# Kernel optimization log

Hardware: AMD Instinct MI355X
Metric: run time of the kernel (lower is better)

## Reference

```python
import jax, jax.numpy as jnp
import numpy as np
import math

D = 768; H = 8; HD = D // H; T = 1024; V = 32000; M = 10
BLOCK = 128          # flex-attention block size (sliding_window_num_blocks granularity)
TAU = 1.0            # gumbel_temp
MAXC = 10            # max middle-block visits == scan length
EPS = 1e-6
IFP = 0.95           # initial_forward_prob

def rms(x):
    return x * jax.lax.rsqrt(jnp.mean(x * x, axis=-1, keepdims=True) + EPS)

def make_rope(t):
    # Rotary.__init__: dim//4 real inv freqs + dim//4 zeros -> cos/sin of shape [t, HD//2]
    inv = (1.0 / 1024) ** jnp.linspace(0.0, 1.0, HD // 4)
    inv = jnp.concatenate([inv, jnp.zeros(HD // 4)])
    th = jnp.arange(t, dtype=jnp.float32)[:, None] * inv[None, :]
    return jnp.cos(th), jnp.sin(th)

def rope(x, cos, sin):
    # x: [1,T,H,HD]
    c = cos[None, :, None, :]; s = sin[None, :, None, :]
    x1, x2 = jnp.split(x, 2, axis=-1)
    return jnp.concatenate([x1 * c + x2 * s, -x1 * s + x2 * c], axis=-1)

def attn(x, ve, wq, wk, wv, wo, lam, cos, sin, mask):
    q = (x @ wq.T).reshape(1, T, H, HD)
    k = (x @ wk.T).reshape(1, T, H, HD)
    v = (x @ wv.T).reshape(1, T, H, HD)
    if ve is not None:
        v = lam[0] * v + lam[1] * ve.reshape(1, T, H, HD)
    else:
        v = lam[0] * v
    q = rope(rms(q), cos, sin); k = rope(rms(k), cos, sin)
    sc = jnp.einsum('bthd,bshd->bhts', q, k) * (1.0 / math.sqrt(HD))
    sc = jnp.where(mask, sc, -1e30)
    y = jnp.einsum('bhts,bshd->bthd', jax.nn.softmax(sc, axis=-1), v).reshape(1, T, D)
    return y @ wo.T

def mlp(x, fc, pr):
    return jnp.square(jax.nn.relu(x @ fc.T)) @ pr.T

def fwd(tokens, embed_w, ve_w, lm_head_w,
        in_wq, in_wk, in_wv, in_wo, in_attn_lam, in_fc, in_pr, in_lam,
        mid_wq, mid_wk, mid_wv, mid_wo, mid_attn_lam, mid_fc, mid_pr, router_w, router_b,
        out_wq, out_wk, out_wv, out_wo, out_attn_lam, out_fc, out_pr, out_lam,
        gumbel_u, window_blocks, max_block_count):
    cos, sin = make_rope(T)
    qi = jnp.arange(T)
    mask = ((qi[:, None] >= qi[None, :]) &
            ((qi[:, None] // BLOCK - qi[None, :] // BLOCK) < window_blocks))[None, None]
    x = rms(embed_w[tokens][None])     # norm(embed(inputs))
    x0 = x
    ve = ve_w[tokens][None]            # X=1 value embedding, reused for output block
    # ---- input FixedBlock ----
    h = in_lam[0] * x + in_lam[1] * x0
    h = h + attn(rms(h), ve, in_wq, in_wk, in_wv, in_wo, in_attn_lam, cos, sin, mask)
    h = h + mlp(rms(h), in_fc, in_pr)
    # ---- middle routing loop (fixed-length scan, masked once exited) ----
    g = -jnp.log(-jnp.log(gumbel_u + 1e-10) + 1e-10)  # [MAXC, M+1] gumbel noise
    mbc = jnp.float32(max_block_count)
    def step(carry, gi):
        x, cur, done, cnt = carry
        y = x + attn(rms(x), None, mid_wq[cur], mid_wk[cur], mid_wv[cur], mid_wo[cur],
                     mid_attn_lam[cur], cos, sin, mask)
        y = y + mlp(rms(y), mid_fc[cur], mid_pr[cur])
        feat = jnp.concatenate([y.mean(axis=1), jnp.stack([cnt, mbc])[None]], axis=-1)  # [1, D+2]
        logits = feat @ router_w[cur].T + router_b[cur]                                  # [1, M+1]
        route = jax.nn.softmax((logits + gi[None]) / TAU, axis=-1)
        nxt = jnp.argmax(route[0]).astype(jnp.int32)
        new_cnt = cnt + 1.0
        exit_now = (nxt == M) | (new_cnt >= mbc)
        x = jnp.where(done, x, y)
        cnt = jnp.where(done, cnt, new_cnt)
        new_done = done | exit_now
        cur = jnp.where(new_done, cur, nxt)
        return (x, cur, new_done, cnt), None
    init = (h, jnp.int32(0), jnp.bool_(False), jnp.float32(0.0))
    (x, _, _, _), _ = jax.lax.scan(step, init, g)
    # ---- output FixedBlock ----
    y = out_lam[0] * x + out_lam[1] * x0
    y = y + attn(rms(y), ve, out_wq, out_wk, out_wv, out_wo, out_attn_lam, cos, sin, mask)
    y = y + mlp(rms(y), out_fc, out_pr)
    logits = rms(y) @ lm_head_w.T
    return 30.0 * jnp.tanh(logits / 30.0)

def setup_inputs() -> dict:
    key = jax.random.key(0)
    ks = iter(jax.random.split(key, 64))
    def w(*s, std=0.02):
        return (std * jax.random.normal(next(ks), s)).astype(jnp.float32)
    rb = np.full((M, M + 1), math.log((1.0 - IFP) / M), dtype=np.float32)
    for i in range(M):
        rb[i, min(i + 1, M)] = math.log(IFP)
    inp = {
        'tokens': jax.random.randint(next(ks), (T,), 0, V, dtype=jnp.int32),
        'embed_w': w(V, D), 've_w': w(V, D), 'lm_head_w': w(V, D),
        'in_wq': w(D, D), 'in_wk': w(D, D), 'in_wv': w(D, D), 'in_wo': w(D, D),
        'in_attn_lam': jnp.array([0.5, 0.5], jnp.float32),
        'in_fc': w(4 * D, D), 'in_pr': w(D, 4 * D),
        'in_lam': jnp.array([1.0, 0.0], jnp.float32),
        'mid_wq': w(M, D, D), 'mid_wk': w(M, D, D), 'mid_wv': w(M, D, D), 'mid_wo': w(M, D, D),
        'mid_attn_lam': jnp.tile(jnp.array([0.5, 0.5], jnp.float32), (M, 1)),
        'mid_fc': w(M, 4 * D, D), 'mid_pr': w(M, D, 4 * D),
        'router_w': w(M, M + 1, D + 2, std=0.001),
        'router_b': jnp.asarray(rb),
        'out_wq': w(D, D), 'out_wk': w(D, D), 'out_wv': w(D, D), 'out_wo': w(D, D),
        'out_attn_lam': jnp.array([0.5, 0.5], jnp.float32),
        'out_fc': w(4 * D, D), 'out_pr': w(D, 4 * D),
        'out_lam': jnp.array([1.0, 0.0], jnp.float32),
        'gumbel_u': jax.random.uniform(next(ks), (MAXC, M + 1), dtype=jnp.float32),
        'window_blocks': 4,
        'max_block_count': MAXC,
    }
    return inp

def reference(tokens, embed_w, ve_w, lm_head_w,
              in_wq, in_wk, in_wv, in_wo, in_attn_lam, in_fc, in_pr, in_lam,
              mid_wq, mid_wk, mid_wv, mid_wo, mid_attn_lam, mid_fc, mid_pr, router_w, router_b,
              out_wq, out_wk, out_wv, out_wo, out_attn_lam, out_fc, out_pr, out_lam,
              gumbel_u, window_blocks, max_block_count):
    return fwd(tokens, embed_w, ve_w, lm_head_w,
               in_wq, in_wk, in_wv, in_wo, in_attn_lam, in_fc, in_pr, in_lam,
               mid_wq, mid_wk, mid_wv, mid_wo, mid_attn_lam, mid_fc, mid_pr, router_w, router_b,
               out_wq, out_wk, out_wv, out_wo, out_attn_lam, out_fc, out_pr, out_lam,
               gumbel_u, window_blocks, max_block_count)
```

## Files before the change

kernel.cpp:

```cpp
#include <hip/hip_runtime.h>
#include <hip/hip_bf16.h>

namespace {

constexpr int cT   = 1024;
constexpr int cD   = 768;
constexpr int cH   = 8;
constexpr int cHD  = 96;
constexpr int cM   = 10;
constexpr int cDff = 3072;
constexpr int cV   = 32000;
constexpr int cTD  = cT * cD;
constexpr float cEps = 1e-6f;

constexpr long oWQ = 0;
constexpr long oWK = 589824;
constexpr long oWV = 2L * 589824;
constexpr long oWO = 3L * 589824;
constexpr long oFC = 4L * 589824;
constexpr long oPR = 4L * 589824 + 2359296;
constexpr long cWTOT = 4L * 589824 + 2L * 2359296;
constexpr int cConvBlocks = (int)(cWTOT / 8 / 256);

typedef __attribute__((ext_vector_type(8))) short short8;
typedef __attribute__((ext_vector_type(4))) float f32x4;

__device__ inline short bf16r(float f) {
  union { float f; unsigned u; } x{f};
  unsigned r = (x.u + 0x7FFF + ((x.u >> 16) & 1)) >> 16;
  return (short)r;
}

__device__ inline float bf2f(short s) {
  union { unsigned u; float f; } x;
  x.u = ((unsigned)(unsigned short)s) << 16;
  return x.f;
}


__global__ void init_state_k(int* cur, int* done, float* cnt, float* feat) {
  if (threadIdx.x == 0) { *cur = 0; *done = 0; *cnt = 0.0f; }
  for (int d = threadIdx.x; d < cD; d += 256) feat[d] = 0.f;
}

__global__ void rope_pre_k(float* __restrict__ cosb, float* __restrict__ sinb) {
  int idx = blockIdx.x * blockDim.x + threadIdx.x;
  if (idx >= cT * 48) return;
  int t = idx / 48, j = idx % 48;
  float th = 0.0f;
  if (j < 24) th = (float)t * powf(1.0f / 1024.0f, (float)j / 23.0f);
  cosb[idx] = cosf(th);
  sinb[idx] = sinf(th);
}

__global__ __launch_bounds__(256) void embed_rms_k(const int* __restrict__ tok,
    const float* __restrict__ ew, const float* __restrict__ vw,
    float* __restrict__ x0, float* __restrict__ ve) {
  int t = blockIdx.x;
  int tk = tok[t];
  const float* er = ew + (size_t)tk * cD;
  const float* vr = vw + (size_t)tk * cD;
  __shared__ float red[256];
  float s = 0.f;
  for (int d = threadIdx.x; d < cD; d += 256) { float e = er[d]; s += e * e; }
  red[threadIdx.x] = s; __syncthreads();
  for (int st = 128; st; st >>= 1) { if (threadIdx.x < st) red[threadIdx.x] += red[threadIdx.x + st]; __syncthreads(); }
  float sc = rsqrtf(red[0] / cD + cEps);
  for (int d = threadIdx.x; d < cD; d += 256) {
    x0[(size_t)t * cD + d] = er[d] * sc;
    ve[(size_t)t * cD + d] = vr[d];
  }
}

__global__ __launch_bounds__(256) void rms_rows_bf(const float* __restrict__ in,
    short* __restrict__ out, const int* done) {
  if (done && *done) return;
  int t = blockIdx.x;
  const float* r = in + (size_t)t * cD;
  __shared__ float red[256];
  float s = 0.f;
  for (int d = threadIdx.x; d < cD; d += 256) { float v = r[d]; s += v * v; }
  red[threadIdx.x] = s; __syncthreads();
  for (int st = 128; st; st >>= 1) { if (threadIdx.x < st) red[threadIdx.x] += red[threadIdx.x + st]; __syncthreads(); }
  float sc = rsqrtf(red[0] / cD + cEps);
  short* o = out + (size_t)t * cD;
  for (int d = threadIdx.x; d < cD; d += 256) o[d] = bf16r(r[d] * sc);
}

__global__ void axpy_lam_k(const float* __restrict__ lam, const float* __restrict__ a,
                           const float* __restrict__ b, float* __restrict__ o, int n) {
  int i = blockIdx.x * 256 + threadIdx.x;
  if (i < n) o[i] = lam[0] * a[i] + lam[1] * b[i];
}


__global__ __launch_bounds__(256) void layer_pre_k(const float* __restrict__ s0,
    const float* __restrict__ s1, const float* __restrict__ s2, const float* __restrict__ s3,
    const float* __restrict__ s4, const float* __restrict__ s5, short* __restrict__ dst,
    const int* __restrict__ cur, const int* __restrict__ done,
    const float* __restrict__ xin, short* __restrict__ xnbf, float* __restrict__ rsum) {
  if (done && *done) return;
  const int b = blockIdx.x;
  if (b < cConvBlocks) {
    long e = ((long)b * 256 + threadIdx.x) * 8;
    long cu = cur ? (long)(*cur) : 0L;
    const float* src;
    if (e < oWK)      src = s0 + cu * 589824  + e;
    else if (e < oWV) src = s1 + cu * 589824  + (e - oWK);
    else if (e < oWO) src = s2 + cu * 589824  + (e - oWV);
    else if (e < oFC) src = s3 + cu * 589824  + (e - oWO);
    else if (e < oPR) src = s4 + cu * 2359296 + (e - oFC);
    else              src = s5 + cu * 2359296 + (e - oPR);
    float4 a0 = *(const float4*)src;
    float4 a1 = *(const float4*)(src + 4);
    short8 sv;
    sv[0]=bf16r(a0.x); sv[1]=bf16r(a0.y); sv[2]=bf16r(a0.z); sv[3]=bf16r(a0.w);
    sv[4]=bf16r(a1.x); sv[5]=bf16r(a1.y); sv[6]=bf16r(a1.z); sv[7]=bf16r(a1.w);
    *(short8*)(dst + e) = sv;
  } else {
    const int t = b - cConvBlocks;
    const float* r = xin + (size_t)t * cD;
    __shared__ float red[256];
    float s = 0.f;
    for (int d = threadIdx.x; d < cD; d += 256) { float v = r[d]; s += v * v; }
    red[threadIdx.x] = s; __syncthreads();
    for (int st = 128; st; st >>= 1) { if (threadIdx.x < st) red[threadIdx.x] += red[threadIdx.x + st]; __syncthreads(); }
    float sc = rsqrtf(red[0] / cD + cEps);
    short* o = xnbf + (size_t)t * cD;
    for (int d = threadIdx.x; d < cD; d += 256) o[d] = bf16r(r[d] * sc);
    if (threadIdx.x == 0) rsum[t] = 0.f;
  }
}

__global__ __launch_bounds__(256) void conv1_k(const float* __restrict__ src,
    short* __restrict__ dst, long nchunk) {
  long i = (long)blockIdx.x * 256 + threadIdx.x;
  if (i >= nchunk) return;
  long e = i * 8;
  float4 a0 = *(const float4*)(src + e);
  float4 a1 = *(const float4*)(src + e + 4);
  short8 sv;
  sv[0]=bf16r(a0.x); sv[1]=bf16r(a0.y); sv[2]=bf16r(a0.z); sv[3]=bf16r(a0.w);
  sv[4]=bf16r(a1.x); sv[5]=bf16r(a1.y); sv[6]=bf16r(a1.z); sv[7]=bf16r(a1.w);
  *(short8*)(dst + e) = sv;
}


__global__ __launch_bounds__(256) void qkv_k(const short* __restrict__ A,
    const short* __restrict__ Wb,
    short* __restrict__ qo, short* __restrict__ ko, short* __restrict__ vo,
    const int* __restrict__ done, const float* __restrict__ lamb,
    const int* __restrict__ cur, const float* __restrict__ vep,
    const float* __restrict__ cosb, const float* __restrict__ sinb) {
  if (done && *done) return;
  const int z = blockIdx.z;
  const short* W = Wb + (long)z * 589824L;
  const int h  = blockIdx.x;
  const int bm = blockIdx.y * 64;
  __shared__ short As[2][64][40];
  __shared__ short Bs[2][96][40];
  const int tid = threadIdx.x;
  const int w = tid >> 6, lane = tid & 63;
  const int fr = lane & 15, fg = lane >> 4;
  const int ar = tid >> 2, ac2 = (tid & 3) << 3;
  const int br1 = (256 + tid) >> 2, bc1 = ((256 + tid) & 3) << 3;

  short8 aN, bN0, bN1;
  aN  = *(const short8*)(A + (size_t)(bm + ar) * cD + ac2);
  bN0 = *(const short8*)(W + (size_t)(h * cHD + ar) * cD + ac2);
  if (tid < 128) bN1 = *(const short8*)(W + (size_t)(h * cHD + br1) * cD + bc1);
  *(short8*)&As[0][ar][ac2] = aN;
  *(short8*)&Bs[0][ar][ac2] = bN0;
  if (tid < 128) *(short8*)&Bs[0][br1][bc1] = bN1;
  __syncthreads();

  f32x4 acc[6] = {};
  int cb = 0;
  for (int kt = 0; kt < cD; kt += 32) {
    const int ktn = kt + 32;
    const bool hn = ktn < cD;
    if (hn) {
      aN  = *(const short8*)(A + (size_t)(bm + ar) * cD + ktn + ac2);
      bN0 = *(const short8*)(W + (size_t)(h * cHD + ar) * cD + ktn + ac2);
      if (tid < 128) bN1 = *(const short8*)(W + (size_t)(h * cHD + br1) * cD + ktn + bc1);
    }
    short8 af = *(const short8*)&As[cb][w * 16 + fr][fg * 8];
#pragma unroll
    for (int n = 0; n < 6; ++n) {
      short8 bf = *(const short8*)&Bs[cb][n * 16 + fr][fg * 8];
      acc[n] = __builtin_amdgcn_mfma_f32_16x16x32_bf16(af, bf, acc[n], 0, 0, 0);
    }
    if (hn) {
      *(short8*)&As[cb ^ 1][ar][ac2] = aN;
      *(short8*)&Bs[cb ^ 1][ar][ac2] = bN0;
      if (tid < 128) *(short8*)&Bs[cb ^ 1][br1][bc1] = bN1;
    }
    __syncthreads();
    cb ^= 1;
  }

  const int t0 = bm + w * 16 + fg * 4;
  if (z < 2) {
    float scl[4];
#pragma unroll
    for (int r = 0; r < 4; ++r) {
      float s = 0.f;
#pragma unroll
      for (int n = 0; n < 6; ++n) s += acc[n][r] * acc[n][r];
#pragma unroll
      for (int mm = 1; mm < 16; mm <<= 1) s += __shfl_xor(s, mm, 64);
      scl[r] = rsqrtf(s * (1.0f / 96.0f) + cEps);
    }
    short* C = (z == 0 ? qo : ko);
#pragma unroll
    for (int r = 0; r < 4; ++r) {
      int t = t0 + r;
      short* orow = C + (size_t)t * cD + h * cHD;
#pragma unroll
      for (int n = 0; n < 3; ++n) {
        int j = n * 16 + fr;
        float c = cosb[t * 48 + j], sn = sinb[t * 48 + j];
        float x1 = acc[n][r] * scl[r], x2 = acc[n + 3][r] * scl[r];
        orow[j]      = bf16r(x1 * c + x2 * sn);
        orow[j + 48] = bf16r(-x1 * sn + x2 * c);
      }
    }
  } else {
    int cu = cur ? *cur : 0;
    float l0 = lamb[2 * cu], l1 = lamb[2 * cu + 1];
#pragma unroll
    for (int r = 0; r < 4; ++r) {
      int t = t0 + r;
#pragma unroll
      for (int n = 0; n < 6; ++n) {
        float val = l0 * acc[n][r];
        if (vep) val += l1 * vep[(size_t)t * cD + h * cHD + n * 16 + fr];
        vo[(size_t)t * cD + h * cHD + n * 16 + fr] = bf16r(val);
      }
    }
  }
}


__global__ __launch_bounds__(256) void attn_f(const short* __restrict__ q,
    const short* __restrict__ k, const short* __restrict__ v, short* __restrict__ o,
    const int* __restrict__ wbp, const int* done) {
  if (done && *done) return;
  const int qb = blockIdx.x;
  const int h  = blockIdx.y;
  const int q0 = qb * 64;
  const int qb128 = q0 >> 7;
  const int wb = *wbp;
  int kb_lo = qb128 - wb + 1; if (kb_lo < 0) kb_lo = 0;

  __shared__ short Ksh[128][136];
  __shared__ short Vt[96][136];

  const int tid  = threadIdx.x;
  const int w    = tid >> 6;
  const int lane = tid & 63;
  const int fr   = lane & 15;
  const int fg   = lane >> 4;

  short8 qf[3];
  {
    const short* qrow = q + (size_t)(q0 + w * 16 + fr) * cD + h * cHD;
#pragma unroll
    for (int ks = 0; ks < 3; ++ks) qf[ks] = *(const short8*)(qrow + ks * 32 + fg * 8);
  }

  short8 rK[6], rV[6];
  auto issue = [&](int kb) {
    const int key0 = kb * 128;
#pragma unroll
    for (int c = 0; c < 6; ++c) {
      int idx = c * 256 + tid;
      int row = idx / 12, colc = (idx % 12) * 8;
      rK[c] = *(const short8*)(k + (size_t)(key0 + row) * cD + h * cHD + colc);
      rV[c] = *(const short8*)(v + (size_t)(key0 + row) * cD + h * cHD + colc);
    }
  };

  f32x4 accO[6] = {};
  float mrun[4], lrun[4];
#pragma unroll
  for (int r = 0; r < 4; ++r) { mrun[r] = -1e30f; lrun[r] = 0.f; }

  issue(kb_lo);
  for (int kb = kb_lo; kb <= qb128; ++kb) {
    __syncthreads();
#pragma unroll
    for (int c = 0; c < 6; ++c) {
      int idx = c * 256 + tid;
      int row = idx / 12, colc = (idx % 12) * 8;
      *(short8*)&Ksh[row][colc] = rK[c];
      short8 vv = rV[c];
#pragma unroll
      for (int i = 0; i < 8; ++i) Vt[colc + i][row] = vv[i];
    }
    __syncthreads();
    if (kb < qb128) issue(kb + 1);

    const int key0 = kb * 128;
    f32x4 s[8];
#pragma unroll
    for (int n = 0; n < 8; ++n) s[n] = (f32x4){0.f, 0.f, 0.f, 0.f};
#pragma unroll
    for (int ks = 0; ks < 3; ++ks) {
#pragma unroll
      for (int n = 0; n < 8; ++n) {
        short8 kf = *(const short8*)&Ksh[n * 16 + fr][ks * 32 + fg * 8];
        s[n] = __builtin_amdgcn_mfma_f32_16x16x32_bf16(qf[ks], kf, s[n], 0, 0, 0);
      }
    }

    float pmax[4] = {-1e30f, -1e30f, -1e30f, -1e30f};
#pragma unroll
    for (int n = 0; n < 8; ++n)
#pragma unroll
      for (int r = 0; r < 4; ++r) {
        float val = s[n][r] * 0.10206207261596577f;
        int key  = key0 + n * 16 + fr;
        int qrow = q0 + w * 16 + fg * 4 + r;
        if (key > qrow) val = -1e30f;
        s[n][r] = val;
        pmax[r] = fmaxf(pmax[r], val);
      }
#pragma unroll
    for (int mm = 1; mm < 16; mm <<= 1)
#pragma unroll
      for (int r = 0; r < 4; ++r) pmax[r] = fmaxf(pmax[r], __shfl_xor(pmax[r], mm, 64));
    float alpha[4], psum[4];
#pragma unroll
    for (int r = 0; r < 4; ++r) {
      float mn = fmaxf(mrun[r], pmax[r]);
      alpha[r] = __expf(mrun[r] - mn);
      mrun[r] = mn;
      psum[r] = 0.f;
    }
#pragma unroll
    for (int n = 0; n < 8; ++n)
#pragma unroll
      for (int r = 0; r < 4; ++r) {
        float p = __expf(s[n][r] - mrun[r]);
        s[n][r] = p;
        psum[r] += p;
      }
#pragma unroll
    for (int mm = 1; mm < 16; mm <<= 1)
#pragma unroll
      for (int r = 0; r < 4; ++r) psum[r] += __shfl_xor(psum[r], mm, 64);
#pragma unroll
    for (int r = 0; r < 4; ++r) lrun[r] = lrun[r] * alpha[r] + psum[r];
#pragma unroll
    for (int n = 0; n < 6; ++n) {
      f32x4 t = accO[n];
#pragma unroll
      for (int r = 0; r < 4; ++r) t[r] *= alpha[r];
      accO[n] = t;
    }

    __syncthreads();
#pragma unroll
    for (int n = 0; n < 8; ++n)
#pragma unroll
      for (int r = 0; r < 4; ++r)
        Ksh[w * 16 + fg * 4 + r][n * 16 + fr] = bf16r(s[n][r]);
    __syncthreads();

#pragma unroll
    for (int ks = 0; ks < 4; ++ks) {
      short8 pf = *(const short8*)&Ksh[w * 16 + fr][ks * 32 + fg * 8];
#pragma unroll
      for (int n = 0; n < 6; ++n) {
        short8 vf = *(const short8*)&Vt[n * 16 + fr][ks * 32 + fg * 8];
        accO[n] = __builtin_amdgcn_mfma_f32_16x16x32_bf16(pf, vf, accO[n], 0, 0, 0);
      }
    }
  }

#pragma unroll
  for (int r = 0; r < 4; ++r) {
    float inv = 1.0f / lrun[r];
    int t = q0 + w * 16 + fg * 4 + r;
#pragma unroll
    for (int n = 0; n < 6; ++n)
      o[(size_t)t * cD + h * cHD + n * 16 + fr] = bf16r(accO[n][r] * inv);
  }
}


template <int EPI, typename OT>
__global__ __launch_bounds__(256) void gemm64_k(const short* __restrict__ A,
    const short* __restrict__ W, OT* __restrict__ C, const int* __restrict__ done,
    const float* __restrict__ res, float* __restrict__ rsum, int ld, int kn, int N) {
  if (done && *done) return;
  const int bm = blockIdx.y * 64;
  const int bn = blockIdx.x * 64;
  const int k0 = blockIdx.z * kn;
  __shared__ short As[2][64][40];
  __shared__ short Bs[2][64][40];
  const int tid = threadIdx.x;
  const int wid = tid >> 6, lane = tid & 63;
  const int wr = wid >> 1, wc = wid & 1;
  const int fr = lane & 15, fg = lane >> 4;
  const int ar = tid >> 2, ac = (tid & 3) << 3;

  short8 aN = *(const short8*)(A + (size_t)(bm + ar) * ld + k0 + ac);
  short8 bN = *(const short8*)(W + (size_t)(bn + ar) * ld + k0 + ac);
  *(short8*)&As[0][ar][ac] = aN;
  *(short8*)&Bs[0][ar][ac] = bN;
  __syncthreads();

  f32x4 acc[2][2] = {};
  int cb = 0;
  for (int kt = 0; kt < kn; kt += 32) {
    const int ktn = kt + 32;
    const bool hn = ktn < kn;
    if (hn) {
      aN = *(const short8*)(A + (size_t)(bm + ar) * ld + k0 + ktn + ac);
      bN = *(const short8*)(W + (size_t)(bn + ar) * ld + k0 + ktn + ac);
    }
    short8 af[2], bfv[2];
#pragma unroll
    for (int m = 0; m < 2; ++m) af[m] = *(const short8*)&As[cb][wr * 32 + m * 16 + fr][fg * 8];
#pragma unroll
    for (int n = 0; n < 2; ++n) bfv[n] = *(const short8*)&Bs[cb][wc * 32 + n * 16 + fr][fg * 8];
#pragma unroll
    for (int m = 0; m < 2; ++m)
#pragma unroll
      for (int n = 0; n < 2; ++n)
        acc[m][n] = __builtin_amdgcn_mfma_f32_16x16x32_bf16(af[m], bfv[n], acc[m][n], 0, 0, 0);
    if (hn) {
      *(short8*)&As[cb ^ 1][ar][ac] = aN;
      *(short8*)&Bs[cb ^ 1][ar][ac] = bN;
    }
    __syncthreads();
    cb ^= 1;
  }
#pragma unroll
  for (int m = 0; m < 2; ++m)
#pragma unroll
    for (int r = 0; r < 4; ++r) {
      const int row = bm + wr * 32 + m * 16 + fg * 4 + r;
      float p = 0.f;
#pragma unroll
      for (int n = 0; n < 2; ++n) {
        const int col = bn + wc * 32 + n * 16 + fr;
        float val = acc[m][n][r];
        if constexpr (EPI == 1) {
          val += res[(size_t)row * N + col];
          C[(size_t)row * N + col] = val;
          p += val * val;
        } else {
          C[(size_t)blockIdx.z * cTD + (size_t)row * N + col] = (OT)bf16r(val);
        }
      }
      if constexpr (EPI == 1) {
#pragma unroll
        for (int mm = 1; mm < 16; mm <<= 1) p += __shfl_xor(p, mm, 64);
        if (fr == 0) atomicAdd(&rsum[row], p);
      }
    }
}


__global__ __launch_bounds__(256) void mgemm_fc_k(const float* __restrict__ Ay,
    const float* __restrict__ rsum, const short* __restrict__ W, short* __restrict__ C,
    const int* __restrict__ done, int K, int N) {
  if (done && *done) return;
  const int bm = blockIdx.y * 64;
  const int bn = blockIdx.x * 64;
  __shared__ short As[2][64][40];
  __shared__ short Bs[2][64][40];
  const int tid = threadIdx.x;
  const int wid = tid >> 6, lane = tid & 63;
  const int wr = wid >> 1, wc = wid & 1;
  const int fr = lane & 15, fg = lane >> 4;
  const int ar = tid >> 2, ac = (tid & 3) << 3;

  const float ascl = rsqrtf(rsum[bm + ar] * (1.0f / cD) + cEps);
  const float* arow = Ay + (size_t)(bm + ar) * K;

  auto loadA = [&](int kt) -> short8 {
    float4 a0 = *(const float4*)(arow + kt + ac);
    float4 a1 = *(const float4*)(arow + kt + ac + 4);
    short8 sv;
    sv[0]=bf16r(a0.x*ascl); sv[1]=bf16r(a0.y*ascl); sv[2]=bf16r(a0.z*ascl); sv[3]=bf16r(a0.w*ascl);
    sv[4]=bf16r(a1.x*ascl); sv[5]=bf16r(a1.y*ascl); sv[6]=bf16r(a1.z*ascl); sv[7]=bf16r(a1.w*ascl);
    return sv;
  };

  short8 aN = loadA(0);
  short8 bN = *(const short8*)(W + (size_t)(bn + ar) * K + ac);
  *(short8*)&As[0][ar][ac] = aN;
  *(short8*)&Bs[0][ar][ac] = bN;
  __syncthreads();

  f32x4 acc[2][2] = {};
  int cb = 0;
  for (int kt = 0; kt < K; kt += 32) {
    const int ktn = kt + 32;
    const bool hn = ktn < K;
    if (hn) {
      aN = loadA(ktn);
      bN = *(const short8*)(W + (size_t)(bn + ar) * K + ktn + ac);
    }
    short8 af[2], bfv[2];
#pragma unroll
    for (int m = 0; m < 2; ++m) af[m] = *(const short8*)&As[cb][wr * 32 + m * 16 + fr][fg * 8];
#pragma unroll
    for (int n = 0; n < 2; ++n) bfv[n] = *(const short8*)&Bs[cb][wc * 32 + n * 16 + fr][fg * 8];
#pragma unroll
    for (int m = 0; m < 2; ++m)
#pragma unroll
      for (int n = 0; n < 2; ++n)
        acc[m][n] = __builtin_amdgcn_mfma_f32_16x16x32_bf16(af[m], bfv[n], acc[m][n], 0, 0, 0);
    if (hn) {
      *(short8*)&As[cb ^ 1][ar][ac] = aN;
      *(short8*)&Bs[cb ^ 1][ar][ac] = bN;
    }
    __syncthreads();
    cb ^= 1;
  }
#pragma unroll
  for (int m = 0; m < 2; ++m)
#pragma unroll
    for (int n = 0; n < 2; ++n)
#pragma unroll
      for (int r = 0; r < 4; ++r) {
        int row = bm + wr * 32 + m * 16 + fg * 4 + r;
        int col = bn + wc * 32 + n * 16 + fr;
        float val = acc[m][n][r];
        val = fmaxf(val, 0.f); val = val * val;
        C[(size_t)row * N + col] = bf16r(val);
      }
}


__global__ __launch_bounds__(256) void reduce_k(const short* __restrict__ pb,
    float* __restrict__ y, float* __restrict__ x, float* __restrict__ feat,
    const int* done) {
  if (done && *done) return;
  __shared__ float red[256];
  const int d = blockIdx.x * 32 + (threadIdx.x & 31);
  const int tc = threadIdx.x >> 5;
  const int t0 = blockIdx.y * 128 + tc * 16;
  float s = 0.f;
  for (int t = t0; t < t0 + 16; ++t) {
    size_t i = (size_t)t * cD + d;
    float v = y[i];
#pragma unroll
    for (int z = 0; z < 4; ++z) v += bf2f(pb[(size_t)z * cTD + i]);
    y[i] = v;
    if (x) x[i] = v;
    s += v;
  }
  if (feat) {
    red[threadIdx.x] = s; __syncthreads();
    if (threadIdx.x < 32) {
      float tot = 0.f;
#pragma unroll
      for (int c = 0; c < 8; ++c) tot += red[c * 32 + threadIdx.x];
      atomicAdd(&feat[d], tot * (1.0f / cT));
    }
  }
}


__global__ void router_step_k(float* __restrict__ feat, const float* __restrict__ rw,
    const float* __restrict__ rb, const float* __restrict__ gu, int iter,
    const int* __restrict__ mbcp, int* cur, int* done, float* cnt) {
  if (*done) return;
  __shared__ float lg[cM + 1];
  const int tid = threadIdx.x;
  const int c = *cur;
  const float mbc = (float)(*mbcp);
  const float cn = *cnt;
  for (int j = 0; j < cM + 1; ++j) {
    const float* w = rw + ((size_t)c * (cM + 1) + j) * (cD + 2);
    float s = 0.f;
    for (int d = tid; d < cD; d += 64) s += feat[d] * w[d];
#pragma unroll
    for (int mm = 32; mm; mm >>= 1) s += __shfl_xor(s, mm, 64);
    if (tid == 0) {
      s += cn * w[cD] + mbc * w[cD + 1] + rb[c * (cM + 1) + j];
      float u = gu[iter * (cM + 1) + j];
      float inner = -logf(u + 1e-10f) + 1e-10f;
      lg[j] = s - logf(inner);
    }
  }
  __syncthreads();
  for (int d = tid; d < cD; d += 64) feat[d] = 0.f;
  if (tid == 0) {
    int nxt = 0; float best = lg[0];
    for (int j = 1; j < cM + 1; ++j) if (lg[j] > best) { best = lg[j]; nxt = j; }
    float nc = cn + 1.0f;
    int ex = (nxt == cM) || (nc >= mbc);
    *cnt = nc;
    if (ex) *done = 1; else *cur = nxt;
  }
}


__global__ __launch_bounds__(256) void gemm_lm_k(const short* __restrict__ A,
    const short* __restrict__ W, float* __restrict__ C) {
  const int nwg = (cV / 128) * (cT / 128);
  const int cpx = nwg / 8;
  const int swz = (blockIdx.x % 8) * cpx + blockIdx.x / 8;
  const int bm = (swz & 7) * 128;
  const int bn = (swz >> 3) * 128;
  __shared__ short As[2][128][40];
  __shared__ short Bs[2][128][40];
  const int tid = threadIdx.x;
  const int wid = tid >> 6, lane = tid & 63;
  const int wr = wid >> 1, wc = wid & 1;
  const int fr = lane & 15, fg = lane >> 4;
  const int r0 = tid >> 2, c0 = (tid & 3) << 3;
  const int r1 = (256 + tid) >> 2, c1 = ((256 + tid) & 3) << 3;

  short8 aN0, aN1, bN0, bN1;
  aN0 = *(const short8*)(A + (size_t)(bm + r0) * cD + c0);
  aN1 = *(const short8*)(A + (size_t)(bm + r1) * cD + c1);
  bN0 = *(const short8*)(W + (size_t)(bn + r0) * cD + c0);
  bN1 = *(const short8*)(W + (size_t)(bn + r1) * cD + c1);
  *(short8*)&As[0][r0][c0] = aN0;
  *(short8*)&As[0][r1][c1] = aN1;
  *(short8*)&Bs[0][r0][c0] = bN0;
  *(short8*)&Bs[0][r1][c1] = bN1;
  __syncthreads();

  f32x4 acc[4][4] = {};
  int cb = 0;
  for (int kt = 0; kt < cD; kt += 32) {
    const int ktn = kt + 32;
    const bool hn = ktn < cD;
    if (hn) {
      aN0 = *(const short8*)(A + (size_t)(bm + r0) * cD + ktn + c0);
      aN1 = *(const short8*)(A + (size_t)(bm + r1) * cD + ktn + c1);
      bN0 = *(const short8*)(W + (size_t)(bn + r0) * cD + ktn + c0);
      bN1 = *(const short8*)(W + (size_t)(bn + r1) * cD + ktn + c1);
    }
    short8 af[4], bfv[4];
#pragma unroll
    for (int m = 0; m < 4; ++m) af[m] = *(const short8*)&As[cb][wr * 64 + m * 16 + fr][fg * 8];
#pragma unroll
    for (int n = 0; n < 4; ++n) bfv[n] = *(const short8*)&Bs[cb][wc * 64 + n * 16 + fr][fg * 8];
#pragma unroll
    for (int m = 0; m < 4; ++m)
#pragma unroll
      for (int n = 0; n < 4; ++n)
        acc[m][n] = __builtin_amdgcn_mfma_f32_16x16x32_bf16(af[m], bfv[n], acc[m][n], 0, 0, 0);
    if (hn) {
      *(short8*)&As[cb ^ 1][r0][c0] = aN0;
      *(short8*)&As[cb ^ 1][r1][c1] = aN1;
      *(short8*)&Bs[cb ^ 1][r0][c0] = bN0;
      *(short8*)&Bs[cb ^ 1][r1][c1] = bN1;
    }
    __syncthreads();
    cb ^= 1;
  }
#pragma unroll
  for (int m = 0; m < 4; ++m)
#pragma unroll
    for (int n = 0; n < 4; ++n)
#pragma unroll
      for (int r = 0; r < 4; ++r) {
        int row = bm + wr * 64 + m * 16 + fg * 4 + r;
        int col = bn + wc * 64 + n * 16 + fr;
        C[(size_t)row * cV + col] = 30.f * tanhf(acc[m][n][r] * (1.f / 30.f));
      }
}

}


extern "C" void kernel_launch(void* const* d_in, const int* in_sizes, int n_in,
                              void* d_out, int out_size, void* d_ws, size_t ws_size,
                              hipStream_t stream) {
  const int*   tokens    = (const int*)d_in[0];
  const float* embed_w   = (const float*)d_in[1];
  const float* ve_w      = (const float*)d_in[2];
  const float* lm_head_w = (const float*)d_in[3];
  const float* in_wq  = (const float*)d_in[4];
  const float* in_wk  = (const float*)d_in[5];
  const float* in_wv  = (const float*)d_in[6];
  const float* in_wo  = (const float*)d_in[7];
  const float* in_al  = (const float*)d_in[8];
  const float* in_fc  = (const float*)d_in[9];
  const float* in_pr  = (const float*)d_in[10];
  const float* in_lam = (const float*)d_in[11];
  const float* mid_wq = (const float*)d_in[12];
  const float* mid_wk = (const float*)d_in[13];
  const float* mid_wv = (const float*)d_in[14];
  const float* mid_wo = (const float*)d_in[15];
  const float* mid_al = (const float*)d_in[16];
  const float* mid_fc = (const float*)d_in[17];
  const float* mid_pr = (const float*)d_in[18];
  const float* router_w = (const float*)d_in[19];
  const float* router_b = (const float*)d_in[20];
  const float* out_wq = (const float*)d_in[21];
  const float* out_wk = (const float*)d_in[22];
  const float* out_wv = (const float*)d_in[23];
  const float* out_wo = (const float*)d_in[24];
  const float* out_al = (const float*)d_in[25];
  const float* out_fc = (const float*)d_in[26];
  const float* out_pr = (const float*)d_in[27];
  const float* out_lam = (const float*)d_in[28];
  const float* gumbel_u = (const float*)d_in[29];
  const int*   wbp  = (const int*)d_in[30];
  const int*   mbcp = (const int*)d_in[31];
  float* outp = (float*)d_out;

  float* ws = (float*)d_ws;
  float* xb   = ws;
  float* x0b  = xb  + cTD;
  float* veb  = x0b + cTD;
  float* yb   = veb + cTD;
  float* cosb = yb  + cTD;
  float* sinb = cosb + cT * 48;
  float* rsum = sinb + cT * 48;
  float* feat = rsum + 1024;
  int*   curp  = (int*)(feat + 784);
  int*   donep = curp + 1;
  float* cntp  = (float*)(curp + 2);
  short* xnbf  = (short*)(feat + 784 + 8);
  short* aobf  = xnbf + cTD;
  short* qbf   = aobf + cTD;
  short* kbf   = qbf  + cTD;
  short* vbf   = kbf  + cTD;
  short* pbuf  = aobf;
  short* hidbf = vbf  + cTD;
  short* wbf   = hidbf + (size_t)cT * cDff;

  const dim3 gPre(cConvBlocks + cT, 1, 1);
  const dim3 gQKV(cH, cT / 64, 3);
  const dim3 gWO(cD / 64, cT / 64, 1);
  const dim3 gPR(cD / 64, cT / 64, 4);
  const dim3 gFF(cDff / 64, cT / 64, 1);
  const dim3 gLM(2000, 1, 1);
  const dim3 gAttn(cT / 64, cH, 1);
  const dim3 gRed(cD / 32, 8, 1);
  const long lmChunks = (long)cV * cD / 8;
  const int gConvLM = (int)(lmChunks / 256);

  auto layer = [&](const float* wq, const float* wk, const float* wv, const float* wo,
                   const float* alam, const float* fc, const float* pr,
                   const int* cur, const int* done,
                   float* xin, float* yout, const float* vept,
                   float* xcom, float* featp) {
    layer_pre_k<<<gPre, 256, 0, stream>>>(wq, wk, wv, wo, fc, pr, wbf, cur, done,
                                          xin, xnbf, rsum);
    qkv_k<<<gQKV, 256, 0, stream>>>(xnbf, wbf, qbf, kbf, vbf, done, alam, cur, vept,
                                    cosb, sinb);
    attn_f<<<gAttn, 256, 0, stream>>>(qbf, kbf, vbf, aobf, wbp, done);
    gemm64_k<1, float><<<gWO, 256, 0, stream>>>(aobf, wbf + oWO, yout, done, xin, rsum,
                                                cD, cD, cD);
    mgemm_fc_k<<<gFF, 256, 0, stream>>>(yout, rsum, wbf + oFC, hidbf, done, cD, cDff);
    gemm64_k<4, short><<<gPR, 256, 0, stream>>>(hidbf, wbf + oPR, pbuf, done, nullptr,
                                                nullptr, cDff, cDff / 4, cD);
    reduce_k<<<gRed, 256, 0, stream>>>(pbuf, yout, xcom, featp, done);
  };

  init_state_k<<<1, 256, 0, stream>>>(curp, donep, cntp, feat);
  rope_pre_k<<<(cT * 48 + 255) / 256, 256, 0, stream>>>(cosb, sinb);
  embed_rms_k<<<cT, 256, 0, stream>>>(tokens, embed_w, ve_w, x0b, veb);

  axpy_lam_k<<<cTD / 256, 256, 0, stream>>>(in_lam, x0b, x0b, xb, cTD);
  layer(in_wq, in_wk, in_wv, in_wo, in_al, in_fc, in_pr, nullptr, nullptr,
        xb, xb, veb, nullptr, nullptr);

  for (int it = 0; it < cM; ++it) {
    layer(mid_wq, mid_wk, mid_wv, mid_wo, mid_al, mid_fc, mid_pr,
          curp, donep, xb, yb, nullptr, xb, feat);
    router_step_k<<<1, 64, 0, stream>>>(feat, router_w, router_b, gumbel_u, it, mbcp,
                                        curp, donep, cntp);
  }

  axpy_lam_k<<<cTD / 256, 256, 0, stream>>>(out_lam, xb, x0b, xb, cTD);
  layer(out_wq, out_wk, out_wv, out_wo, out_al, out_fc, out_pr, nullptr, nullptr,
        xb, xb, veb, nullptr, nullptr);

  conv1_k<<<gConvLM, 256, 0, stream>>>(lm_head_w, wbf, lmChunks);
  rms_rows_bf<<<cT, 256, 0, stream>>>(xb, xnbf, nullptr);
  gemm_lm_k<<<gLM, 256, 0, stream>>>(xnbf, wbf, outp);
}
```

Before: 2.126 ms.

## Move WO/FC/PR weight conversion into attention kernel as extra blocks

Weight fp32->bf16 conversion for the WO, FC and PR matrices is moved out of the layer prologue kernel and into extra blocks appended to the attention launch grid. Only the QKV weights are still converted before the QKV GEMM. The aim is to shorten the critical path before qkv_k and let the bandwidth-bound conversion overlap with the compute-bound attention blocks. The risk is that the extra blocks compete with attention for CUs and that the grid sizing (324 x 8 blocks) has to cover the remaining chunks exactly.

```diff
diff --git a/kernel.cpp b/kernel.cpp
--- a/kernel.cpp
+++ b/kernel.cpp
@@ -20,7 +20,8 @@
 constexpr long oFC = 4L * 589824;
 constexpr long oPR = 4L * 589824 + 2359296;
 constexpr long cWTOT = 4L * 589824 + 2L * 2359296;
-constexpr int cConvBlocks = (int)(cWTOT / 8 / 256);
+constexpr int cConvQKV  = (int)(3L * 589824 / 2048);
+constexpr int cConvRest = (int)((cWTOT - oWO) / 2048);
 
 typedef __attribute__((ext_vector_type(8))) short short8;
 typedef __attribute__((ext_vector_type(4))) float f32x4;
@@ -35,6 +36,15 @@
   union { unsigned u; float f; } x;
   x.u = ((unsigned)(unsigned short)s) << 16;
   return x.f;
+}
+
+__device__ inline void cvtstore8(const float* __restrict__ src, short* __restrict__ dst) {
+  float4 a0 = *(const float4*)src;
+  float4 a1 = *(const float4*)(src + 4);
+  short8 sv;
+  sv[0]=bf16r(a0.x); sv[1]=bf16r(a0.y); sv[2]=bf16r(a0.z); sv[3]=bf16r(a0.w);
+  sv[4]=bf16r(a1.x); sv[5]=bf16r(a1.y); sv[6]=bf16r(a1.z); sv[7]=bf16r(a1.w);
+  *(short8*)dst = sv;
 }
 
 
@@ -95,30 +105,21 @@
 
 
 __global__ __launch_bounds__(256) void layer_pre_k(const float* __restrict__ s0,
-    const float* __restrict__ s1, const float* __restrict__ s2, const float* __restrict__ s3,
-    const float* __restrict__ s4, const float* __restrict__ s5, short* __restrict__ dst,
+    const float* __restrict__ s1, const float* __restrict__ s2, short* __restrict__ dst,
     const int* __restrict__ cur, const int* __restrict__ done,
     const float* __restrict__ xin, short* __restrict__ xnbf, float* __restrict__ rsum) {
   if (done && *done) return;
   const int b = blockIdx.x;
-  if (b < cConvBlocks) {
+  if (b < cConvQKV) {
     long e = ((long)b * 256 + threadIdx.x) * 8;
     long cu = cur ? (long)(*cur) : 0L;
     const float* src;
-    if (e < oWK)      src = s0 + cu * 589824  + e;
-    else if (e < oWV) src = s1 + cu * 589824  + (e - oWK);
-    else if (e < oWO) src = s2 + cu * 589824  + (e - oWV);
-    else if (e < oFC) src = s3 + cu * 589824  + (e - oWO);
-    else if (e < oPR) src = s4 + cu * 2359296 + (e - oFC);
-    else              src = s5 + cu * 2359296 + (e - oPR);
-    float4 a0 = *(const float4*)src;
-    float4 a1 = *(const float4*)(src + 4);
-    short8 sv;
-    sv[0]=bf16r(a0.x); sv[1]=bf16r(a0.y); sv[2]=bf16r(a0.z); sv[3]=bf16r(a0.w);
-    sv[4]=bf16r(a1.x); sv[5]=bf16r(a1.y); sv[6]=bf16r(a1.z); sv[7]=bf16r(a1.w);
-    *(short8*)(dst + e) = sv;
+    if (e < oWK)      src = s0 + cu * 589824L + e;
+    else if (e < oWV) src = s1 + cu * 589824L + (e - oWK);
+    else              src = s2 + cu * 589824L + (e - oWV);
+    cvtstore8(src, dst + e);
   } else {
-    const int t = b - cConvBlocks;
+    const int t = b - cConvQKV;
     const float* r = xin + (size_t)t * cD;
     __shared__ float red[256];
     float s = 0.f;
@@ -137,12 +138,7 @@
   long i = (long)blockIdx.x * 256 + threadIdx.x;
   if (i >= nchunk) return;
   long e = i * 8;
-  float4 a0 = *(const float4*)(src + e);
-  float4 a1 = *(const float4*)(src + e + 4);
-  short8 sv;
-  sv[0]=bf16r(a0.x); sv[1]=bf16r(a0.y); sv[2]=bf16r(a0.z); sv[3]=bf16r(a0.w);
-  sv[4]=bf16r(a1.x); sv[5]=bf16r(a1.y); sv[6]=bf16r(a1.z); sv[7]=bf16r(a1.w);
-  *(short8*)(dst + e) = sv;
+  cvtstore8(src + e, dst + e);
 }
 
 
@@ -244,8 +240,23 @@
 
 __global__ __launch_bounds__(256) void attn_f(const short* __restrict__ q,
     const short* __restrict__ k, const short* __restrict__ v, short* __restrict__ o,
-    const int* __restrict__ wbp, const int* done) {
+    const int* __restrict__ wbp, const int* done,
+    const float* __restrict__ s3, const float* __restrict__ s4,
+    const float* __restrict__ s5, const int* __restrict__ cur,
+    short* __restrict__ wdst) {
   if (done && *done) return;
+  if (blockIdx.x >= cT / 64) {
+    long cb = (long)(blockIdx.x - cT / 64) * gridDim.y + blockIdx.y;
+    if (cb >= cConvRest) return;
+    long e = oWO + (cb * 256 + threadIdx.x) * 8;
+    long cu = cur ? (long)(*cur) : 0L;
+    const float* src;
+    if (e < oFC)      src = s3 + cu * 589824L + (e - oWO);
+    else if (e < oPR) src = s4 + cu * 2359296L + (e - oFC);
+    else              src = s5 + cu * 2359296L + (e - oPR);
+    cvtstore8(src, wdst + e);
+    return;
+  }
   const int qb = blockIdx.x;
   const int h  = blockIdx.y;
   const int q0 = qb * 64;
@@ -733,13 +744,13 @@
   short* hidbf = vbf  + cTD;
   short* wbf   = hidbf + (size_t)cT * cDff;
 
-  const dim3 gPre(cConvBlocks + cT, 1, 1);
+  const dim3 gPre(cConvQKV + cT, 1, 1);
   const dim3 gQKV(cH, cT / 64, 3);
   const dim3 gWO(cD / 64, cT / 64, 1);
   const dim3 gPR(cD / 64, cT / 64, 4);
   const dim3 gFF(cDff / 64, cT / 64, 1);
   const dim3 gLM(2000, 1, 1);
-  const dim3 gAttn(cT / 64, cH, 1);
+  const dim3 gAttn(cT / 64 + 324, cH, 1);
   const dim3 gRed(cD / 32, 8, 1);
   const long lmChunks = (long)cV * cD / 8;
   const int gConvLM = (int)(lmChunks / 256);
@@ -749,11 +760,12 @@
                    const int* cur, const int* done,
                    float* xin, float* yout, const float* vept,
                    float* xcom, float* featp) {
-    layer_pre_k<<<gPre, 256, 0, stream>>>(wq, wk, wv, wo, fc, pr, wbf, cur, done,
+    layer_pre_k<<<gPre, 256, 0, stream>>>(wq, wk, wv, wbf, cur, done,
                                           xin, xnbf, rsum);
     qkv_k<<<gQKV, 256, 0, stream>>>(xnbf, wbf, qbf, kbf, vbf, done, alam, cur, vept,
                                     cosb, sinb);
-    attn_f<<<gAttn, 256, 0, stream>>>(qbf, kbf, vbf, aobf, wbp, done);
+    attn_f<<<gAttn, 256, 0, stream>>>(qbf, kbf, vbf, aobf, wbp, done,
+                                      wo, fc, pr, cur, wbf);
     gemm64_k<1, float><<<gWO, 256, 0, stream>>>(aobf, wbf + oWO, yout, done, xin, rsum,
                                                 cD, cD, cD);
     mgemm_fc_k<<<gFF, 256, 0, stream>>>(yout, rsum, wbf + oFC, hidbf, done, cD, cDff);
```

Result: slower. 2.234 ms (+5.1%).
